# Kernel optimization log

Hardware: AMD Instinct MI355X
Metric: run time of the kernel (lower is better)

The kernel has to match this reference:

```python
import jax, jax.numpy as jnp
import numpy as np

B, S, HID = 1, 2048, 2048
NH, NKV, HD = 32, 8, 64
INTER = 8192
EPS = 1e-6


def rmsnorm(x, w, eps=EPS):
    xf = x.astype(jnp.float32)
    inv = jax.lax.rsqrt(jnp.mean(xf * xf, axis=-1, keepdims=True) + eps)
    return (xf * inv * w).astype(x.dtype)


def rope(x, sin_t, cos_t):
    # x: [B, S, H, D]; sin/cos: [S, D//2]
    sin = sin_t[None, :, None, :]
    cos = cos_t[None, :, None, :]
    d2 = x.shape[-1] // 2
    x0, x1 = x[..., :d2], x[..., d2:]
    return jnp.concatenate((x0 * cos - x1 * sin, x0 * sin + x1 * cos), axis=-1)


def setup_inputs() -> dict:
    key = jax.random.key(0)
    ks = jax.random.split(key, 12)
    hidden_states = jax.random.normal(ks[0], (B, S, HID), dtype=jnp.float32)
    # realistic RoPE tables
    inv_freq = 1.0 / (10000.0 ** (np.arange(0, HD // 2, dtype=np.float32) * 2.0 / HD))
    ang = np.arange(S, dtype=np.float32)[:, None] * inv_freq[None, :]
    sin_table = jnp.asarray(np.sin(ang))
    cos_table = jnp.asarray(np.cos(ang))
    s = 0.02
    return {
        "hidden_states": hidden_states,
        "sin_table": sin_table,
        "cos_table": cos_table,
        "ln1_w": jnp.ones((HID,), jnp.float32),
        "ln2_w": jnp.ones((HID,), jnp.float32),
        "wq": jax.random.normal(ks[1], (HID, NH * HD), jnp.float32) * s,
        "wk": jax.random.normal(ks[2], (HID, NKV * HD), jnp.float32) * s,
        "wv": jax.random.normal(ks[3], (HID, NKV * HD), jnp.float32) * s,
        "wo": jax.random.normal(ks[4], (NH * HD, HID), jnp.float32) * s,
        "w_gate": jax.random.normal(ks[5], (HID, INTER), jnp.float32) * s,
        "w_up": jax.random.normal(ks[6], (HID, INTER), jnp.float32) * s,
        "w_down": jax.random.normal(ks[7], (INTER, HID), jnp.float32) * s,
    }


def attention(x, sin_t, cos_t, wq, wk, wv, wo):
    b, s, _ = x.shape
    q = (x @ wq).reshape(b, s, NH, HD)
    k = (x @ wk).reshape(b, s, NKV, HD)
    v = (x @ wv).reshape(b, s, NKV, HD).transpose(0, 2, 1, 3)  # [B,Hk,S,D]
    q = rope(q, sin_t, cos_t).transpose(0, 2, 1, 3)  # [B,Hq,S,D]
    k = rope(k, sin_t, cos_t).transpose(0, 2, 1, 3)  # [B,Hk,S,D]
    g = NH // NKV
    k = jnp.repeat(k, g, axis=1)
    v = jnp.repeat(v, g, axis=1)
    scale = 1.0 / np.sqrt(HD)
    scores = jnp.einsum("bhqd,bhkd->bhqk", q, k) * scale
    mask = jnp.tril(jnp.ones((s, s), dtype=bool))
    scores = jnp.where(mask, scores, -jnp.inf)
    probs = jax.nn.softmax(scores, axis=-1)
    out = jnp.einsum("bhqk,bhkd->bhqd", probs, v)
    out = out.transpose(0, 2, 1, 3).reshape(b, s, NH * HD)
    return out @ wo


def reference(hidden_states, sin_table, cos_table, ln1_w, ln2_w, wq, wk, wv, wo, w_gate, w_up, w_down):
    x = hidden_states
    x = x + attention(rmsnorm(x, ln1_w), sin_table, cos_table, wq, wk, wv, wo)
    h = rmsnorm(x, ln2_w)
    x = x + (jax.nn.silu(h @ w_gate) * (h @ w_up)) @ w_down
    return x
```

## Files before the change

### kernel.cpp

```cpp
#include <hip/hip_runtime.h>
#include <hip/hip_bf16.h>

typedef float f32x4 __attribute__((ext_vector_type(4)));
typedef unsigned int u32x4 __attribute__((ext_vector_type(4)));
typedef unsigned short u16;

#define S_LEN 2048
#define HID 2048
#define NHEAD 32
#define NKVH 8
#define HDIM 64

__device__ __forceinline__ unsigned short f2bf_bits(float f) {
    unsigned int u = __builtin_bit_cast(unsigned int, f);
    unsigned int r = u + 0x7fffu + ((u >> 16) & 1u);
    return (unsigned short)(r >> 16);
}
__device__ __forceinline__ float bf2f(unsigned short b) {
    unsigned int u = ((unsigned int)b) << 16;
    return __builtin_bit_cast(float, u);
}

__device__ __forceinline__ f32x4 mfma_bf16(u32x4 a, u32x4 b, f32x4 c) {
    asm("v_mfma_f32_16x16x32_bf16 %0, %1, %2, %0" : "+v"(c) : "v"(a), "v"(b));
    return c;
}

__device__ __forceinline__ void gload_lds16(const void* g, void* l) {
    __builtin_amdgcn_global_load_lds(
        (const __attribute__((address_space(1))) void*)g,
        (__attribute__((address_space(3))) void*)l, 16, 0, 0);
}

__global__ __launch_bounds__(256)
void rmsnorm_k(const float* __restrict__ x, const float* __restrict__ wgt,
               unsigned short* __restrict__ out)
{
    int row = blockIdx.x;
    int t = threadIdx.x;
    const float* xr = x + (size_t)row * HID;
    f32x4 a = *(const f32x4*)(xr + t * 8);
    f32x4 b = *(const f32x4*)(xr + t * 8 + 4);
    float s = 0.f;
#pragma unroll
    for (int i = 0; i < 4; ++i) s += a[i] * a[i] + b[i] * b[i];
#pragma unroll
    for (int off = 32; off > 0; off >>= 1) s += __shfl_down(s, off);
    __shared__ float red[4];
    if ((t & 63) == 0) red[t >> 6] = s;
    __syncthreads();
    float tot = red[0] + red[1] + red[2] + red[3];
    float inv = rsqrtf(tot * (1.0f / (float)HID) + 1e-6f);
    f32x4 wa = *(const f32x4*)(wgt + t * 8);
    f32x4 wb = *(const f32x4*)(wgt + t * 8 + 4);
    unsigned int pk[4];
#pragma unroll
    for (int i = 0; i < 2; ++i) {
        pk[i]     = (unsigned)f2bf_bits(a[2*i] * inv * wa[2*i]) |
                    ((unsigned)f2bf_bits(a[2*i+1] * inv * wa[2*i+1]) << 16);
        pk[i + 2] = (unsigned)f2bf_bits(b[2*i] * inv * wb[2*i]) |
                    ((unsigned)f2bf_bits(b[2*i+1] * inv * wb[2*i+1]) << 16);
    }
    u32x4 ov; ov[0] = pk[0]; ov[1] = pk[1]; ov[2] = pk[2]; ov[3] = pk[3];
    *(u32x4*)(out + (size_t)row * HID + t * 8) = ov;
}

__global__ __launch_bounds__(256)
void transpose_cvt(const float* __restrict__ in, unsigned short* __restrict__ out,
                   int K, int N)
{
    __shared__ unsigned short tile[64 * 65];
    int kb = blockIdx.y * 64, nb = blockIdx.x * 64;
    int t = threadIdx.x;
    int r = t >> 2, c0 = (t & 3) * 16;
    const float* src = in + (size_t)(kb + r) * N + nb + c0;
#pragma unroll
    for (int j = 0; j < 4; ++j) {
        f32x4 v = *(const f32x4*)(src + j * 4);
#pragma unroll
        for (int i = 0; i < 4; ++i)
            tile[r * 65 + c0 + j * 4 + i] = f2bf_bits(v[i]);
    }
    __syncthreads();
    unsigned short e[16];
#pragma unroll
    for (int j = 0; j < 16; ++j) e[j] = tile[(c0 + j) * 65 + r];
    u32x4 o0, o1;
#pragma unroll
    for (int j = 0; j < 4; ++j) {
        o0[j] = (unsigned)e[2*j] | ((unsigned)e[2*j+1] << 16);
        o1[j] = (unsigned)e[8 + 2*j] | ((unsigned)e[8 + 2*j+1] << 16);
    }
    unsigned short* dst = out + (size_t)(nb + r) * K + kb + c0;
    *(u32x4*)(dst) = o0;
    *(u32x4*)(dst + 8) = o1;
}

__global__ __launch_bounds__(256)
void rope_k(unsigned short* __restrict__ qkv, const float* __restrict__ sin_t,
            const float* __restrict__ cos_t)
{
    int s = blockIdx.x;
    for (int it = threadIdx.x; it < (NHEAD + NKVH) * 32; it += 256) {
        int slot = it >> 5;
        int d = it & 31;
        int col = (slot < NHEAD) ? slot * 64 + d : HID + (slot - NHEAD) * 64 + d;
        unsigned short* p = qkv + (size_t)s * 3072 + col;
        float x0 = bf2f(p[0]);
        float x1 = bf2f(p[32]);
        float c = cos_t[s * 32 + d];
        float sn = sin_t[s * 32 + d];
        p[0]  = f2bf_bits(x0 * c - x1 * sn);
        p[32] = f2bf_bits(x0 * sn + x1 * c);
    }
}

__global__ __launch_bounds__(256)
void transpose_v(const unsigned short* __restrict__ qkv, unsigned short* __restrict__ vT)
{
    __shared__ unsigned short tile[64][80];
    int kb = blockIdx.x * 64, kvh = blockIdx.y;
    int t = threadIdx.x;
    int r = t >> 2, c0 = (t & 3) * 16;
    const unsigned short* src = qkv + (size_t)(kb + r) * 3072 + 2560 + kvh * 64 + c0;
    u32x4 v0 = *(const u32x4*)(src);
    u32x4 v1 = *(const u32x4*)(src + 8);
    *(u32x4*)&tile[r][c0] = v0;
    *(u32x4*)&tile[r][c0 + 8] = v1;
    __syncthreads();
    int d = t >> 2, k0 = (t & 3) * 16;
    unsigned short e[16];
#pragma unroll
    for (int j = 0; j < 16; ++j) e[j] = tile[k0 + j][d];
    u32x4 o0, o1;
#pragma unroll
    for (int j = 0; j < 4; ++j) {
        o0[j] = (unsigned)e[2*j] | ((unsigned)e[2*j+1] << 16);
        o1[j] = (unsigned)e[8 + 2*j] | ((unsigned)e[8 + 2*j+1] << 16);
    }
    int s0 = ((k0 >> 3) ^ (d & 7)) & 7;
    int s1 = (((k0 >> 3) + 1) ^ (d & 7)) & 7;
    unsigned short* dst = vT + ((size_t)kvh * 64 + d) * 2048 + kb;
    *(u32x4*)(dst + s0 * 8) = o0;
    *(u32x4*)(dst + s1 * 8) = o1;
}

template <int EPI>
__global__ __launch_bounds__(256)
void gemm_bt(const unsigned short* __restrict__ A,
             const unsigned short* __restrict__ Bt,
             void* __restrict__ outp, const void* __restrict__ auxp,
             int M, int N, int Kc, int lda)
{
    __shared__ unsigned short As[2][128 * 32];
    __shared__ unsigned short Bs[2][128 * 32];
    int t = threadIdx.x, w = t >> 6, l = t & 63;
    int rb = blockIdx.y, cb = blockIdx.x, zb = blockIdx.z;
    int wr = w >> 1, wc = w & 1;
    int l4 = l >> 4, l15 = l & 15;
    int arow = l >> 2, acol = (l & 3) * 8;
    f32x4 acc[4][4] = {};
    const unsigned short* Ag = A + (size_t)rb * 128 * lda + (size_t)zb * Kc
                                 + (size_t)(w * 16 + arow) * lda + acol;
    const unsigned short* Bg = Bt + (size_t)cb * 128 * lda + (size_t)zb * Kc
                                 + (size_t)(w * 16 + arow) * lda + acol;
    int nk = Kc >> 5;

#define STAGE(buf, kt)                                                          \
    {                                                                           \
        const unsigned short* Agk = Ag + (size_t)(kt) * 32;                     \
        const unsigned short* Bgk = Bg + (size_t)(kt) * 32;                     \
        gload_lds16(Agk, &As[buf][w * 512]);                                    \
        gload_lds16(Agk + (size_t)64 * lda, &As[buf][(4 + w) * 512]);           \
        gload_lds16(Bgk, &Bs[buf][w * 512]);                                    \
        gload_lds16(Bgk + (size_t)64 * lda, &Bs[buf][(4 + w) * 512]);           \
    }

    STAGE(0, 0);
    __syncthreads();
    int cur = 0;
    for (int kt = 0; kt < nk; ++kt) {
        if (kt + 1 < nk) STAGE(cur ^ 1, kt + 1);
        u32x4 af[4], bfr[4];
#pragma unroll
        for (int i = 0; i < 4; ++i)
            af[i] = *(const u32x4*)(&As[cur][(wr * 64 + i * 16 + l15) * 32 + l4 * 8]);
#pragma unroll
        for (int n = 0; n < 4; ++n)
            bfr[n] = *(const u32x4*)(&Bs[cur][(wc * 64 + n * 16 + l15) * 32 + l4 * 8]);
#pragma unroll
        for (int i = 0; i < 4; ++i)
#pragma unroll
            for (int n = 0; n < 4; ++n)
                acc[i][n] = mfma_bf16(af[i], bfr[n], acc[i][n]);
        __syncthreads();
        cur ^= 1;
    }
#undef STAGE

    int row0 = rb * 128 + wr * 64 + l4 * 4;
    int col0 = cb * 128 + wc * 64 + l15;
#pragma unroll
    for (int i = 0; i < 4; ++i) {
#pragma unroll
        for (int n = 0; n < 4; ++n) {
#pragma unroll
            for (int r = 0; r < 4; ++r) {
                int row = row0 + i * 16 + r;
                int col = col0 + n * 16;
                size_t idx = (size_t)row * N + col;
                float v = acc[i][n][r];
                if (EPI == 0) {
                    ((unsigned short*)outp)[idx] = f2bf_bits(v);
                } else if (EPI == 3) {
                    ((float*)outp)[idx] = v + ((const float*)auxp)[idx];
                } else {
                    ((float*)outp)[(size_t)zb * M * N + idx] = v;
                }
            }
        }
    }
}

template <int KK, int QUAD, int WAITN>
__device__ __forceinline__ void phase8(u16* lds, int cur, f32x4 (&acc)[8][4],
                                       int aoff, int boff,
                                       const u16* Asrc, const u16* Bsrc,
                                       int K, int kt_next, bool dostage,
                                       int dst0, int dst1)
{
    const u16* ah = lds + (cur * 4 + KK * 2) * 8192 + aoff + QUAD * 2048;
    const u16* bh = lds + (cur * 4 + KK * 2 + 1) * 8192 + boff;
    u32x4 af[4], bfv[4];
#pragma unroll
    for (int mi = 0; mi < 4; ++mi) af[mi] = *(const u32x4*)(ah + mi * 512);
#pragma unroll
    for (int ni = 0; ni < 4; ++ni) bfv[ni] = *(const u32x4*)(bh + ni * 512);
    if (dostage) {
        const u16* src = (QUAD ? Bsrc : Asrc) + (size_t)kt_next * 64 + KK * 32;
        u16* d = lds + ((cur ^ 1) * 4 + (KK * 2 + QUAD)) * 8192;
        gload_lds16(src, d + dst0);
        gload_lds16(src + (size_t)128 * K, d + dst1);
    }
    __builtin_amdgcn_s_barrier();
    __builtin_amdgcn_s_setprio(1);
#pragma unroll
    for (int mi = 0; mi < 4; ++mi)
#pragma unroll
        for (int ni = 0; ni < 4; ++ni)
            acc[QUAD * 4 + mi][ni] = mfma_bf16(af[mi], bfv[ni], acc[QUAD * 4 + mi][ni]);
    __builtin_amdgcn_s_setprio(0);
    if (WAITN == 4) asm volatile("s_waitcnt vmcnt(4)" ::: "memory");
    else if (WAITN == 0) asm volatile("s_waitcnt vmcnt(0)" ::: "memory");
    __builtin_amdgcn_s_barrier();
}

template <int EPI>
__global__ __launch_bounds__(512, 2)
void gemm8p(const u16* __restrict__ A, const u16* __restrict__ Bt,
            void* __restrict__ outp, const void* __restrict__ auxp,
            int M, int N, int K)
{
    extern __shared__ u16 lds[];
    const int tid = threadIdx.x;
    const int w = tid >> 6, l = tid & 63;
    const int wm = w >> 2, wn = w & 3;
    const int l4 = l >> 4, l15 = l & 15;

    int wg = blockIdx.x, nwg = gridDim.x;
    int swzb = ((nwg & 7) == 0) ? ((wg & 7) * (nwg >> 3) + (wg >> 3)) : wg;
    int rbs = M >> 8;
    int rb = swzb % rbs, cb = swzb / rbs;

    const int sw = ((tid & 3) ^ ((tid >> 3) & 3)) * 8;
    const int srow = tid >> 2;
    const u16* Asrc = A + (size_t)(rb * 256 + srow) * K + sw;
    const u16* Bsrc = Bt + (size_t)(cb * 256 + srow) * K + sw;
    const int dst0 = tid * 8, dst1 = (512 + tid) * 8;

    const int rswz = (l15 >> 1) & 3;
    const int aoff = (wm * 128 + l15) * 32 + (l4 ^ rswz) * 8;
    const int boff = (wn * 64 + l15) * 32 + (l4 ^ rswz) * 8;

    f32x4 acc[8][4] = {};
    const int NT = K >> 6;

#pragma unroll
    for (int h = 0; h < 2; ++h) {
        const u16* sA = Asrc + h * 32;
        const u16* sB = Bsrc + h * 32;
        gload_lds16(sA, lds + (h * 2) * 8192 + dst0);
        gload_lds16(sA + (size_t)128 * K, lds + (h * 2) * 8192 + dst1);
        gload_lds16(sB, lds + (h * 2 + 1) * 8192 + dst0);
        gload_lds16(sB + (size_t)128 * K, lds + (h * 2 + 1) * 8192 + dst1);
    }
    asm volatile("s_waitcnt vmcnt(4)" ::: "memory");
    __builtin_amdgcn_s_barrier();

    for (int t = 0; t < NT - 1; ++t) {
        int cur = t & 1;
        phase8<0, 0, -1>(lds, cur, acc, aoff, boff, Asrc, Bsrc, K, t + 1, true, dst0, dst1);
        phase8<0, 1,  4>(lds, cur, acc, aoff, boff, Asrc, Bsrc, K, t + 1, true, dst0, dst1);
        phase8<1, 0, -1>(lds, cur, acc, aoff, boff, Asrc, Bsrc, K, t + 1, true, dst0, dst1);
        phase8<1, 1,  4>(lds, cur, acc, aoff, boff, Asrc, Bsrc, K, t + 1, true, dst0, dst1);
    }
    {
        int cur = (NT - 1) & 1;
        phase8<0, 0, -1>(lds, cur, acc, aoff, boff, Asrc, Bsrc, K, 0, false, dst0, dst1);
        phase8<0, 1,  0>(lds, cur, acc, aoff, boff, Asrc, Bsrc, K, 0, false, dst0, dst1);
        phase8<1, 0, -1>(lds, cur, acc, aoff, boff, Asrc, Bsrc, K, 0, false, dst0, dst1);
        phase8<1, 1, -1>(lds, cur, acc, aoff, boff, Asrc, Bsrc, K, 0, false, dst0, dst1);
    }

    int row0 = rb * 256 + wm * 128 + l4 * 4;
    int col0 = cb * 256 + wn * 64 + l15;
#pragma unroll
    for (int mi = 0; mi < 8; ++mi) {
#pragma unroll
        for (int ni = 0; ni < 4; ++ni) {
#pragma unroll
            for (int r = 0; r < 4; ++r) {
                int row = row0 + mi * 16 + r;
                int col = col0 + ni * 16;
                size_t idx = (size_t)row * N + col;
                float v = acc[mi][ni][r];
                if (EPI == 1) {
                    float sv = v / (1.0f + __expf(-v));
                    ((unsigned short*)outp)[idx] = f2bf_bits(sv);
                } else {
                    float gv = bf2f(((const unsigned short*)auxp)[idx]);
                    ((unsigned short*)outp)[idx] = f2bf_bits(v * gv);
                }
            }
        }
    }
}

__global__ __launch_bounds__(256)
void reduce_add2(float* __restrict__ out, const float* __restrict__ p, int n)
{
    int i = (blockIdx.x * 256 + threadIdx.x) * 4;
    f32x4 a = *(const f32x4*)(out + i);
    f32x4 b = *(const f32x4*)(p + i);
    f32x4 c = *(const f32x4*)(p + (size_t)n + i);
    a = a + b + c;
    *(f32x4*)(out + i) = a;
}

__global__ __launch_bounds__(256)
void attn_fwd(const unsigned short* __restrict__ qkv,
              const unsigned short* __restrict__ vT,
              unsigned short* __restrict__ out)
{
    int p = blockIdx.x, h = blockIdx.y, kvh = h >> 2;
    int t = threadIdx.x, w = t >> 6, l = t & 63;
    int l4 = l >> 4, l15 = l & 15;
    __shared__ unsigned short Ks[2][64 * 64];
    __shared__ unsigned short Vs[2][64 * 64];
    __shared__ unsigned short Pl[4][16 * 72];
    unsigned short* Pw = &Pl[w][0];

    const unsigned short* Kg = qkv + HID + kvh * 64;
    const unsigned short* Vg = vT + (size_t)kvh * 64 * 2048;

    int ch0 = w * 2, ch1 = w * 2 + 1;
    int rsub = l >> 3;
    int ksw = ((l & 7) ^ (rsub & 7)) * 8;
    int vcol = (l & 7) * 8;
    int sw0 = (l4 ^ (l15 & 7)) * 8;
    int sw1 = ((l4 | 4) ^ (l15 & 7)) * 8;

#define STAGE_KV(buf, kt)                                                         \
    {                                                                             \
        gload_lds16(Kg + (size_t)((kt) * 64 + ch0 * 8 + rsub) * 3072 + ksw,       \
                    &Ks[buf][ch0 * 512]);                                         \
        gload_lds16(Kg + (size_t)((kt) * 64 + ch1 * 8 + rsub) * 3072 + ksw,       \
                    &Ks[buf][ch1 * 512]);                                         \
        gload_lds16(Vg + (size_t)(ch0 * 8 + rsub) * 2048 + (kt) * 64 + vcol,      \
                    &Vs[buf][ch0 * 512]);                                         \
        gload_lds16(Vg + (size_t)(ch1 * 8 + rsub) * 2048 + (kt) * 64 + vcol,      \
                    &Vs[buf][ch1 * 512]);                                         \
    }

    const float SC2 = 0.18033688f;
    const float THR = 44.36f;
    const float BIG = -3.0e38f;

    for (int half = 0; half < 2; ++half) {
        int qb = half ? (31 - p) : p;
        int qrow0 = qb * 64 + w * 16;
        STAGE_KV(0, 0);
        const unsigned short* qg = qkv + (size_t)(qrow0 + l15) * 3072 + h * 64 + l4 * 8;
        u32x4 aq0 = *(const u32x4*)(qg);
        u32x4 aq1 = *(const u32x4*)(qg + 32);
        f32x4 o[4] = {};
        float m[4], ls[4] = {};
#pragma unroll
        for (int r = 0; r < 4; ++r) m[r] = BIG;
        __syncthreads();
        int cur = 0;
        for (int kt = 0; kt <= qb; ++kt) {
            if (kt < qb) STAGE_KV(cur ^ 1, kt + 1);
            f32x4 sc[4];
#pragma unroll
            for (int n = 0; n < 4; ++n) {
                const unsigned short* kb_ = &Ks[cur][(n * 16 + l15) * 64];
                u32x4 b0 = *(const u32x4*)(kb_ + sw0);
                u32x4 b1 = *(const u32x4*)(kb_ + sw1);
                f32x4 z = {};
                z = mfma_bf16(aq0, b0, z);
                z = mfma_bf16(aq1, b1, z);
                sc[n] = z;
            }
            if (kt == qb) {
#pragma unroll
                for (int n = 0; n < 4; ++n) {
                    int kcol = n * 16 + l15;
#pragma unroll
                    for (int r = 0; r < 4; ++r) {
                        int qr = w * 16 + l4 * 4 + r;
                        if (kcol > qr) sc[n][r] = BIG;
                    }
                }
            }
            float rmax[4];
#pragma unroll
            for (int r = 0; r < 4; ++r)
                rmax[r] = fmaxf(fmaxf(sc[0][r], sc[1][r]), fmaxf(sc[2][r], sc[3][r]));
#pragma unroll
            for (int msk = 1; msk <= 8; msk <<= 1)
#pragma unroll
                for (int r = 0; r < 4; ++r)
                    rmax[r] = fmaxf(rmax[r], __shfl_xor(rmax[r], msk));
            float need = 0.f;
#pragma unroll
            for (int r = 0; r < 4; ++r) need = fmaxf(need, rmax[r] - m[r]);
            if (__ballot(need > THR)) {
#pragma unroll
                for (int r = 0; r < 4; ++r) {
                    float mn = fmaxf(m[r], rmax[r]);
                    float al = __builtin_exp2f((m[r] - mn) * SC2);
                    m[r] = mn;
                    ls[r] *= al;
#pragma unroll
                    for (int nd = 0; nd < 4; ++nd) o[nd][r] *= al;
                }
            }
            float rs[4] = {}, ms[4];
#pragma unroll
            for (int r = 0; r < 4; ++r) ms[r] = m[r] * SC2;
#pragma unroll
            for (int n = 0; n < 4; ++n)
#pragma unroll
                for (int r = 0; r < 4; ++r) {
                    float pe = __builtin_exp2f(__builtin_fmaf(sc[n][r], SC2, -ms[r]));
                    sc[n][r] = pe;
                    rs[r] += pe;
                }
#pragma unroll
            for (int msk = 1; msk <= 8; msk <<= 1)
#pragma unroll
                for (int r = 0; r < 4; ++r) rs[r] += __shfl_xor(rs[r], msk);
#pragma unroll
            for (int r = 0; r < 4; ++r) ls[r] += rs[r];
#pragma unroll
            for (int n = 0; n < 4; ++n)
#pragma unroll
                for (int r = 0; r < 4; ++r)
                    Pw[(l4 * 4 + r) * 72 + n * 16 + l15] = f2bf_bits(sc[n][r]);
            asm volatile("s_waitcnt lgkmcnt(0)" ::: "memory");
            __builtin_amdgcn_sched_barrier(0);
            u32x4 ap0 = *(const u32x4*)(Pw + l15 * 72 + l4 * 8);
            u32x4 ap1 = *(const u32x4*)(Pw + l15 * 72 + 32 + l4 * 8);
#pragma unroll
            for (int nd = 0; nd < 4; ++nd) {
                const unsigned short* vb = &Vs[cur][(nd * 16 + l15) * 64];
                u32x4 bv0 = *(const u32x4*)(vb + sw0);
                u32x4 bv1 = *(const u32x4*)(vb + sw1);
                o[nd] = mfma_bf16(ap0, bv0, o[nd]);
                o[nd] = mfma_bf16(ap1, bv1, o[nd]);
            }
            __syncthreads();
            cur ^= 1;
        }
#undef STAGE_KV
        float linv[4];
#pragma unroll
        for (int r = 0; r < 4; ++r) linv[r] = 1.0f / ls[r];
#pragma unroll
        for (int nd = 0; nd < 4; ++nd)
#pragma unroll
            for (int r = 0; r < 4; ++r)
                out[(size_t)(qrow0 + l4 * 4 + r) * HID + h * 64 + nd * 16 + l15] =
                    f2bf_bits(o[nd][r] * linv[r]);
    }
}

extern "C" void kernel_launch(void* const* d_in, const int* in_sizes, int n_in,
                              void* d_out, int out_size, void* d_ws, size_t ws_size,
                              hipStream_t stream)
{
    const float* x     = (const float*)d_in[0];
    const float* sin_t = (const float*)d_in[1];
    const float* cos_t = (const float*)d_in[2];
    const float* ln1w  = (const float*)d_in[3];
    const float* ln2w  = (const float*)d_in[4];
    const float* wq    = (const float*)d_in[5];
    const float* wk    = (const float*)d_in[6];
    const float* wv    = (const float*)d_in[7];
    const float* wo    = (const float*)d_in[8];
    const float* wg    = (const float*)d_in[9];
    const float* wu    = (const float*)d_in[10];
    const float* wd    = (const float*)d_in[11];
    float* out = (float*)d_out;

    char* ws = (char*)d_ws;
    if (ws_size < 113246208u) return;
    unsigned short* wT   = (unsigned short*)(ws);
    unsigned short* xn   = (unsigned short*)(ws + 33554432u);
    unsigned short* qkv  = (unsigned short*)(ws + 41943040u);
    unsigned short* attn = (unsigned short*)(ws + 54525952u);
    unsigned short* vT   = (unsigned short*)(ws + 62914560u);
    float*          part = (float*)(ws + 33554432u);
    unsigned short* g    = (unsigned short*)(ws + 79691776u);

    hipFuncSetAttribute(reinterpret_cast<const void*>(&gemm8p<1>),
                        hipFuncAttributeMaxDynamicSharedMemorySize, 131072);
    hipFuncSetAttribute(reinterpret_cast<const void*>(&gemm8p<2>),
                        hipFuncAttributeMaxDynamicSharedMemorySize, 131072);

    rmsnorm_k<<<S_LEN, 256, 0, stream>>>(x, ln1w, xn);

    transpose_cvt<<<dim3(32, 32), 256, 0, stream>>>(wq, wT, 2048, 2048);
    transpose_cvt<<<dim3(8, 32), 256, 0, stream>>>(wk, wT + (size_t)2048 * 2048, 2048, 512);
    transpose_cvt<<<dim3(8, 32), 256, 0, stream>>>(wv, wT + (size_t)2560 * 2048, 2048, 512);

    gemm_bt<0><<<dim3(24, 16, 1), 256, 0, stream>>>(xn, wT, qkv, nullptr, 2048, 3072, 2048, 2048);

    rope_k<<<S_LEN, 256, 0, stream>>>(qkv, sin_t, cos_t);
    transpose_v<<<dim3(32, 8), 256, 0, stream>>>(qkv, vT);

    attn_fwd<<<dim3(16, 32), 256, 0, stream>>>(qkv, vT, attn);

    transpose_cvt<<<dim3(32, 32), 256, 0, stream>>>(wo, wT, 2048, 2048);
    gemm_bt<3><<<dim3(16, 16, 1), 256, 0, stream>>>(attn, wT, out, x, 2048, 2048, 2048, 2048);

    rmsnorm_k<<<S_LEN, 256, 0, stream>>>(out, ln2w, xn);

    transpose_cvt<<<dim3(128, 32), 256, 0, stream>>>(wg, wT, 2048, 8192);
    gemm8p<1><<<dim3(256), 512, 131072, stream>>>(xn, wT, g, nullptr, 2048, 8192, 2048);

    transpose_cvt<<<dim3(128, 32), 256, 0, stream>>>(wu, wT, 2048, 8192);
    gemm8p<2><<<dim3(256), 512, 131072, stream>>>(xn, wT, g, g, 2048, 8192, 2048);

    transpose_cvt<<<dim3(32, 128), 256, 0, stream>>>(wd, wT, 8192, 2048);
    gemm_bt<4><<<dim3(16, 16, 2), 256, 0, stream>>>(g, wT, part, nullptr, 2048, 2048, 4096, 8192);

    reduce_add2<<<4096, 256, 0, stream>>>(out, part, 4194304);
}
```

Baseline: 499.1 us.

## Split down-projection K four ways with fp16 partials; reuse B fragments across quads

The down-projection GEMM is split-K over four slices instead of two, which doubles the number of workgroups. Each slice writes its partial sums as fp16 rather than fp32 to cut workspace traffic, and the reduction kernel sums four fp16 partials into the fp32 output. The gemm8p kernel now loads the B fragments from LDS only in the first quad phase and reuses them in the second. It also adds an explicit lgkmcnt wait and a sched_barrier before the MFMAs. Storing fp16 partials costs some accuracy and could overflow on large values.

```diff
diff --git a/kernel.cpp b/kernel.cpp
--- a/kernel.cpp
+++ b/kernel.cpp
@@ -3,6 +3,7 @@
 
 typedef float f32x4 __attribute__((ext_vector_type(4)));
 typedef unsigned int u32x4 __attribute__((ext_vector_type(4)));
+typedef _Float16 f16x4 __attribute__((ext_vector_type(4)));
 typedef unsigned short u16;
 
 #define S_LEN 2048
@@ -215,7 +216,7 @@
                 } else if (EPI == 3) {
                     ((float*)outp)[idx] = v + ((const float*)auxp)[idx];
                 } else {
-                    ((float*)outp)[(size_t)zb * M * N + idx] = v;
+                    ((_Float16*)outp)[(size_t)zb * M * N + idx] = (_Float16)v;
                 }
             }
         }
@@ -224,18 +225,21 @@
 
 template <int KK, int QUAD, int WAITN>
 __device__ __forceinline__ void phase8(u16* lds, int cur, f32x4 (&acc)[8][4],
+                                       u32x4 (&bfv)[4],
                                        int aoff, int boff,
                                        const u16* Asrc, const u16* Bsrc,
                                        int K, int kt_next, bool dostage,
                                        int dst0, int dst1)
 {
     const u16* ah = lds + (cur * 4 + KK * 2) * 8192 + aoff + QUAD * 2048;
-    const u16* bh = lds + (cur * 4 + KK * 2 + 1) * 8192 + boff;
-    u32x4 af[4], bfv[4];
+    u32x4 af[4];
 #pragma unroll
     for (int mi = 0; mi < 4; ++mi) af[mi] = *(const u32x4*)(ah + mi * 512);
-#pragma unroll
-    for (int ni = 0; ni < 4; ++ni) bfv[ni] = *(const u32x4*)(bh + ni * 512);
+    if (QUAD == 0) {
+        const u16* bh = lds + (cur * 4 + KK * 2 + 1) * 8192 + boff;
+#pragma unroll
+        for (int ni = 0; ni < 4; ++ni) bfv[ni] = *(const u32x4*)(bh + ni * 512);
+    }
     if (dostage) {
         const u16* src = (QUAD ? Bsrc : Asrc) + (size_t)kt_next * 64 + KK * 32;
         u16* d = lds + ((cur ^ 1) * 4 + (KK * 2 + QUAD)) * 8192;
@@ -243,6 +247,8 @@
         gload_lds16(src + (size_t)128 * K, d + dst1);
     }
     __builtin_amdgcn_s_barrier();
+    asm volatile("s_waitcnt lgkmcnt(0)" ::: "memory");
+    __builtin_amdgcn_sched_barrier(0);
     __builtin_amdgcn_s_setprio(1);
 #pragma unroll
     for (int mi = 0; mi < 4; ++mi)
@@ -283,6 +289,7 @@
     const int boff = (wn * 64 + l15) * 32 + (l4 ^ rswz) * 8;
 
     f32x4 acc[8][4] = {};
+    u32x4 bfv[4];
     const int NT = K >> 6;
 
 #pragma unroll
@@ -299,17 +306,17 @@
 
     for (int t = 0; t < NT - 1; ++t) {
         int cur = t & 1;
-        phase8<0, 0, -1>(lds, cur, acc, aoff, boff, Asrc, Bsrc, K, t + 1, true, dst0, dst1);
-        phase8<0, 1,  4>(lds, cur, acc, aoff, boff, Asrc, Bsrc, K, t + 1, true, dst0, dst1);
-        phase8<1, 0, -1>(lds, cur, acc, aoff, boff, Asrc, Bsrc, K, t + 1, true, dst0, dst1);
-        phase8<1, 1,  4>(lds, cur, acc, aoff, boff, Asrc, Bsrc, K, t + 1, true, dst0, dst1);
+        phase8<0, 0, -1>(lds, cur, acc, bfv, aoff, boff, Asrc, Bsrc, K, t + 1, true, dst0, dst1);
+        phase8<0, 1,  4>(lds, cur, acc, bfv, aoff, boff, Asrc, Bsrc, K, t + 1, true, dst0, dst1);
+        phase8<1, 0, -1>(lds, cur, acc, bfv, aoff, boff, Asrc, Bsrc, K, t + 1, true, dst0, dst1);
+        phase8<1, 1,  4>(lds, cur, acc, bfv, aoff, boff, Asrc, Bsrc, K, t + 1, true, dst0, dst1);
     }
     {
         int cur = (NT - 1) & 1;
-        phase8<0, 0, -1>(lds, cur, acc, aoff, boff, Asrc, Bsrc, K, 0, false, dst0, dst1);
-        phase8<0, 1,  0>(lds, cur, acc, aoff, boff, Asrc, Bsrc, K, 0, false, dst0, dst1);
-        phase8<1, 0, -1>(lds, cur, acc, aoff, boff, Asrc, Bsrc, K, 0, false, dst0, dst1);
-        phase8<1, 1, -1>(lds, cur, acc, aoff, boff, Asrc, Bsrc, K, 0, false, dst0, dst1);
+        phase8<0, 0, -1>(lds, cur, acc, bfv, aoff, boff, Asrc, Bsrc, K, 0, false, dst0, dst1);
+        phase8<0, 1,  0>(lds, cur, acc, bfv, aoff, boff, Asrc, Bsrc, K, 0, false, dst0, dst1);
+        phase8<1, 0, -1>(lds, cur, acc, bfv, aoff, boff, Asrc, Bsrc, K, 0, false, dst0, dst1);
+        phase8<1, 1, -1>(lds, cur, acc, bfv, aoff, boff, Asrc, Bsrc, K, 0, false, dst0, dst1);
     }
 
     int row0 = rb * 256 + wm * 128 + l4 * 4;
@@ -337,13 +344,16 @@
 }
 
 __global__ __launch_bounds__(256)
-void reduce_add2(float* __restrict__ out, const float* __restrict__ p, int n)
+void reduce_add4(float* __restrict__ out, const _Float16* __restrict__ p, int n)
 {
     int i = (blockIdx.x * 256 + threadIdx.x) * 4;
     f32x4 a = *(const f32x4*)(out + i);
-    f32x4 b = *(const f32x4*)(p + i);
-    f32x4 c = *(const f32x4*)(p + (size_t)n + i);
-    a = a + b + c;
+#pragma unroll
+    for (int z = 0; z < 4; ++z) {
+        f16x4 h = *(const f16x4*)(p + (size_t)z * n + i);
+#pragma unroll
+        for (int j = 0; j < 4; ++j) a[j] += (float)h[j];
+    }
     *(f32x4*)(out + i) = a;
 }
 
@@ -521,7 +531,7 @@
     unsigned short* qkv  = (unsigned short*)(ws + 41943040u);
     unsigned short* attn = (unsigned short*)(ws + 54525952u);
     unsigned short* vT   = (unsigned short*)(ws + 62914560u);
-    float*          part = (float*)(ws + 33554432u);
+    _Float16*       part = (_Float16*)(ws + 33554432u);
     unsigned short* g    = (unsigned short*)(ws + 79691776u);
 
     hipFuncSetAttribute(reinterpret_cast<const void*>(&gemm8p<1>),
@@ -554,7 +564,7 @@
     gemm8p<2><<<dim3(256), 512, 131072, stream>>>(xn, wT, g, g, 2048, 8192, 2048);
 
     transpose_cvt<<<dim3(32, 128), 256, 0, stream>>>(wd, wT, 8192, 2048);
-    gemm_bt<4><<<dim3(16, 16, 2), 256, 0, stream>>>(g, wT, part, nullptr, 2048, 2048, 4096, 8192);
-
-    reduce_add2<<<4096, 256, 0, stream>>>(out, part, 4194304);
-}
+    gemm_bt<5><<<dim3(16, 16, 4), 256, 0, stream>>>(g, wT, part, nullptr, 2048, 2048, 2048, 8192);
+
+    reduce_add4<<<4096, 256, 0, stream>>>(out, part, 4194304);
+}
```

Result: faster. 485.2 us (-2.8%).
